# Performance work log

Hardware: AMD Instinct MI355X
Metric: run time of the kernel (lower is better)

Reference implementation:

```python
import jax, jax.numpy as jnp
import numpy as np
import math

B, S, D, H, K = 8, 4096, 1024, 16, 256
DK = D // H


def setup_inputs() -> dict:
    key = jax.random.key(0)
    ks = jax.random.split(key, 8)
    s = 1.0 / math.sqrt(D)
    x = jax.random.normal(ks[0], (B, S, D), dtype=jnp.float32)
    Wq = jax.random.normal(ks[1], (D, D), dtype=jnp.float32) * s
    Wk = jax.random.normal(ks[2], (D, D), dtype=jnp.float32) * s
    Wv = jax.random.normal(ks[3], (D, D), dtype=jnp.float32) * s
    Wo = jax.random.normal(ks[4], (D, D), dtype=jnp.float32) * s
    bq = jnp.zeros((D,), jnp.float32)
    bk = jnp.zeros((D,), jnp.float32)
    bv = jnp.zeros((D,), jnp.float32)
    bo = jnp.zeros((D,), jnp.float32)
    # xavier-uniform-style scale for the low-rank projections
    lim = math.sqrt(6.0 / (S + K))
    E = jax.random.uniform(ks[5], (S, K), jnp.float32, -lim, lim)
    Fp = jax.random.uniform(ks[6], (S, K), jnp.float32, -lim, lim)
    return {"x": x, "Wq": Wq, "bq": bq, "Wk": Wk, "bk": bk,
            "Wv": Wv, "bv": bv, "Wo": Wo, "bo": bo, "E": E, "Fp": Fp}


def reference(x, Wq, bq, Wk, bk, Wv, bv, Wo, bo, E, Fp):
    b, s, d = x.shape
    # QKV projections, split heads: [b, h, s, dk]
    def heads(y):
        return y.reshape(b, s, H, DK).transpose(0, 2, 1, 3)
    Q = heads(x @ Wq + bq)
    Kh = heads(x @ Wk + bk)
    Vh = heads(x @ Wv + bv)
    # Low-rank projection of K, V along sequence: [b, h, k, dk]
    Kp = jnp.einsum('sk,bhsd->bhkd', E, Kh)
    Vp = jnp.einsum('sk,bhsd->bhkd', Fp, Vh)
    # Attention over projected length k
    scores = jnp.einsum('bhsd,bhkd->bhsk', Q, Kp) / math.sqrt(DK)
    attn = jax.nn.softmax(scores, axis=-1)
    out = jnp.einsum('bhsk,bhkd->bhsd', attn, Vp)
    out = out.transpose(0, 2, 1, 3).reshape(b, s, d)
    return out @ Wo + bo
```

## Files before the change

### kernel.cpp

```cpp
#include <hip/hip_runtime.h>

#define AS1 __attribute__((address_space(1)))
#define AS3 __attribute__((address_space(3)))

typedef __attribute__((ext_vector_type(8))) short s16x8;
typedef __attribute__((ext_vector_type(4))) float f32x4;
typedef __attribute__((ext_vector_type(4))) unsigned short u16x4;
typedef __attribute__((ext_vector_type(8))) unsigned short u16x8;

#define MFMA16(a, b, c) __builtin_amdgcn_mfma_f32_16x16x32_bf16(a, b, c, 0, 0, 0)

static __device__ __forceinline__ unsigned short f2bf(float f) {
  unsigned u = __builtin_bit_cast(unsigned, f);
  u += 0x7fffu + ((u >> 16) & 1u);
  return (unsigned short)(u >> 16);
}

static __device__ __forceinline__ void gll16(const unsigned short* g, char* l) {
  __builtin_amdgcn_global_load_lds((const AS1 void*)g, (AS3 void*)l, 16, 0, 0);
}

#define BAR() asm volatile("s_barrier" ::: "memory")
#define WAITV(N) asm volatile("s_waitcnt vmcnt(" #N ")" ::: "memory")
#define FENCE() asm volatile("" ::: "memory")

__device__ __forceinline__ void gemm256_pipe(const unsigned short* __restrict__ A0, int lda,
                                             const unsigned short* __restrict__ B0, int ldb,
                                             int NT2, char* lds, f32x4 (&acc)[8][4]) {
  const int t = threadIdx.x;
  const int lane = t & 63, w = t >> 6, g = lane >> 4, l15 = lane & 15;
  const int wm = w >> 2, wn = w & 3;
  char* const A_lds[2] = {lds, lds + 65536};
  char* const B_lds[2] = {lds + 32768, lds + 98304};
  s16x8 af[2][4], bfr[2][4];

  const int rl = t >> 3, sl = t & 7;
  const unsigned short* aB = A0 + (size_t)rl * lda + ((sl ^ (rl & 7)) << 3);
  const unsigned short* bB = B0 + (size_t)rl * ldb + ((sl ^ (rl & 7)) << 3);
  const int woff = w << 10;

  char* pA[2][2];
  char* pB[2][2];
#pragma unroll
  for (int b = 0; b < 2; ++b)
#pragma unroll
    for (int kk = 0; kk < 2; ++kk) {
      pA[b][kk] = lds + b * 65536 + (wm * 64 + l15) * 128 + (((kk * 4 + g) ^ (l15 & 7)) << 4);
      pB[b][kk] = lds + 32768 + b * 65536 + (wn * 32 + l15) * 128 + (((kk * 4 + g) ^ (l15 & 7)) << 4);
    }

#define STGA(BUF, H, PTR)                                                                \
  do {                                                                                   \
    gll16((PTR) + (size_t)((H)*128) * lda, A_lds[BUF] + woff + (H)*16384);               \
    gll16((PTR) + (size_t)((H)*128 + 64) * lda, A_lds[BUF] + woff + (H)*16384 + 8192);   \
  } while (0)
#define STGB(BUF, H, PTR)                                                                \
  do {                                                                                   \
    gll16((PTR) + (size_t)((H)*128) * ldb, B_lds[BUF] + woff + (H)*16384);               \
    gll16((PTR) + (size_t)((H)*128 + 64) * ldb, B_lds[BUF] + woff + (H)*16384 + 8192);   \
  } while (0)

#define LDAQ(BUF, QH)                                                                    \
  do {                                                                                   \
    _Pragma("unroll") for (int mi = 0; mi < 4; ++mi)                                     \
        _Pragma("unroll") for (int kk = 0; kk < 2; ++kk)                                 \
            af[kk][mi] = *(const s16x8*)(pA[BUF][kk] + (QH)*16384 + mi * 2048);          \
  } while (0)
#define LDBP(BUF, NH)                                                                    \
  do {                                                                                   \
    _Pragma("unroll") for (int ni = 0; ni < 2; ++ni)                                     \
        _Pragma("unroll") for (int kk = 0; kk < 2; ++kk)                                 \
            bfr[kk][(NH)*2 + ni] =                                                       \
                *(const s16x8*)(pB[BUF][kk] + (NH)*16384 + ni * 2048);                   \
  } while (0)
#define MQUAD(QH, NH)                                                                    \
  do {                                                                                   \
    __builtin_amdgcn_s_setprio(1);                                                       \
    _Pragma("unroll") for (int kk = 0; kk < 2; ++kk)                                     \
        _Pragma("unroll") for (int mi = 0; mi < 4; ++mi)                                 \
            _Pragma("unroll") for (int ni = 0; ni < 2; ++ni)                             \
                acc[(QH)*4 + mi][(NH)*2 + ni] =                                          \
        MFMA16(af[kk][mi], bfr[kk][(NH)*2 + ni], acc[(QH)*4 + mi][(NH)*2 + ni]);         \
    __builtin_amdgcn_s_setprio(0);                                                       \
  } while (0)

  STGA(0, 0, aB);
  STGB(0, 0, bB);
  STGB(0, 1, bB);
  STGA(0, 1, aB);
  STGA(1, 0, aB + 64);
  STGB(1, 0, bB + 64);
  STGB(1, 1, bB + 64);
  STGA(1, 1, aB + 64);
  WAITV(8);
  BAR();

  for (int it = 0; it < NT2; ++it) {
    const bool pf = (it + 1 < NT2);
    const unsigned short* aN = aB + it * 128 + 128;
    const unsigned short* bN = bB + it * 128 + 128;
    LDAQ(0, 0);
    LDBP(0, 0);
    MQUAD(0, 0);
    BAR();
    LDBP(0, 1);
    if (pf) { STGA(0, 0, aN); STGB(0, 0, bN); }
    MQUAD(0, 1);
    BAR();
    LDAQ(0, 1);
    if (pf) STGB(0, 1, bN);
    MQUAD(1, 0);
    BAR();
    if (pf) STGA(0, 1, aN);
    MQUAD(1, 1);
    if (pf) WAITV(8);
    else WAITV(0);
    BAR();
    LDAQ(1, 0);
    LDBP(1, 0);
    MQUAD(0, 0);
    BAR();
    LDBP(1, 1);
    if (pf) { STGA(1, 0, aN + 64); STGB(1, 0, bN + 64); }
    MQUAD(0, 1);
    BAR();
    LDAQ(1, 1);
    if (pf) STGB(1, 1, bN + 64);
    MQUAD(1, 0);
    BAR();
    if (pf) STGA(1, 1, aN + 64);
    MQUAD(1, 1);
    if (pf) WAITV(8);
    BAR();
  }
#undef STGA
#undef STGB
#undef LDAQ
#undef LDBP
#undef MQUAD
}

__global__ __launch_bounds__(512, 2) void k_gemm_q(const unsigned short* __restrict__ xb,
                                                   const unsigned short* __restrict__ Wqt,
                                                   const float* __restrict__ biasq,
                                                   unsigned short* __restrict__ Qb) {
  __shared__ __align__(16) char lds[131072];
  f32x4 acc[8][4];
#pragma unroll
  for (int i = 0; i < 8; ++i)
#pragma unroll
    for (int j = 0; j < 4; ++j) acc[i][j] = f32x4{0.f, 0.f, 0.f, 0.f};
  int bid = blockIdx.y * 4 + blockIdx.x;
  bid = (bid & 7) * 64 + (bid >> 3);
  const int bn = bid & 3, bm = bid >> 2;
  gemm256_pipe(xb + (size_t)bm * 256 * 1024, 1024, Wqt + (size_t)bn * 256 * 1024, 1024, 8, lds, acc);

  const int t = threadIdx.x, lane = t & 63, w = t >> 6, g = lane >> 4, l15 = lane & 15;
  const int wm = w >> 2, wn = w & 3;
  const float QSC = 0.1803368801111204f;
#pragma unroll
  for (int nf = 0; nf < 4; ++nf) {
    const int n = bn * 256 + (nf >> 1) * 128 + wn * 32 + (nf & 1) * 16 + l15;
    const float bias = biasq[n];
#pragma unroll
    for (int mq = 0; mq < 8; ++mq) {
      const int m0 = bm * 256 + (mq >> 2) * 128 + wm * 64 + (mq & 3) * 16 + g * 4;
      const f32x4 v = acc[mq][nf];
#pragma unroll
      for (int r = 0; r < 4; ++r) Qb[(size_t)(m0 + r) * 1024 + n] = f2bf((v[r] + bias) * QSC);
    }
  }
}

__global__ __launch_bounds__(512, 2) void k_gemm_out(const unsigned short* __restrict__ AO,
                                                     const unsigned short* __restrict__ Wot,
                                                     const float* __restrict__ bo,
                                                     float* __restrict__ out) {
  __shared__ __align__(16) char lds[131072];
  f32x4 acc[8][4];
#pragma unroll
  for (int i = 0; i < 8; ++i)
#pragma unroll
    for (int j = 0; j < 4; ++j) acc[i][j] = f32x4{0.f, 0.f, 0.f, 0.f};
  int bid = blockIdx.y * 4 + blockIdx.x;
  bid = (bid & 7) * 64 + (bid >> 3);
  const int bn = bid & 3, bm = bid >> 2;
  gemm256_pipe(AO + (size_t)bm * 256 * 1024, 1024, Wot + (size_t)bn * 256 * 1024, 1024, 8, lds, acc);

  const int t = threadIdx.x, lane = t & 63, w = t >> 6, g = lane >> 4, l15 = lane & 15;
  const int wm = w >> 2, wn = w & 3;
#pragma unroll
  for (int nf = 0; nf < 4; ++nf) {
    const int n = bn * 256 + (nf >> 1) * 128 + wn * 32 + (nf & 1) * 16 + l15;
    const float bias = bo[n];
#pragma unroll
    for (int mq = 0; mq < 8; ++mq) {
      const int m0 = bm * 256 + (mq >> 2) * 128 + wm * 64 + (mq & 3) * 16 + g * 4;
      const f32x4 v = acc[mq][nf];
#pragma unroll
      for (int r = 0; r < 4; ++r) out[(size_t)(m0 + r) * 1024 + n] = v[r] + bias;
    }
  }
}

__device__ __forceinline__ void gemm_tile(const unsigned short* __restrict__ Ab, int lda,
                                          const unsigned short* __restrict__ Bb, int ldb,
                                          int Kc, char* lds, f32x4 (&acc)[4][4]) {
  const int t = threadIdx.x;
  const int lane = t & 63, w = t >> 6, g = lane >> 4, l15 = lane & 15;
  const int wm = w >> 1, wn = w & 1;
  char* As = lds;
  char* Bs = lds + 16384;
  for (int ks = 0; ks < Kc; ks += 64) {
    __syncthreads();
#pragma unroll
    for (int i = 0; i < 4; ++i) {
      const int c = i * 256 + t, row = c >> 3, sl = c & 7;
      const int col = ks + ((sl ^ (row & 7)) << 3);
      const int ubase = (i * 256 + w * 64) << 4;
      gll16(Ab + (size_t)row * lda + col, As + ubase);
      gll16(Bb + (size_t)row * ldb + col, Bs + ubase);
    }
    __syncthreads();
    s16x8 af[2][4], bfr[2][4];
#pragma unroll
    for (int kk = 0; kk < 2; ++kk)
#pragma unroll
      for (int x4 = 0; x4 < 4; ++x4) {
        const int ra = wm * 64 + x4 * 16 + l15;
        const int rb = wn * 64 + x4 * 16 + l15;
        af[kk][x4] = *(const s16x8*)(As + ra * 128 + ((((kk << 2) + g) ^ (ra & 7)) << 4));
        bfr[kk][x4] = *(const s16x8*)(Bs + rb * 128 + ((((kk << 2) + g) ^ (rb & 7)) << 4));
      }
#pragma unroll
    for (int kk = 0; kk < 2; ++kk)
#pragma unroll
      for (int mt = 0; mt < 4; ++mt)
#pragma unroll
        for (int nt = 0; nt < 4; ++nt)
          acc[mt][nt] = MFMA16(af[kk][mt], bfr[kk][nt], acc[mt][nt]);
  }
}

__global__ __launch_bounds__(256) void k_gemm_xef(const unsigned short* __restrict__ Et,
                                                  const unsigned short* __restrict__ Ft,
                                                  const unsigned short* __restrict__ xbT,
                                                  float* __restrict__ pxef) {
  __shared__ __align__(16) char lds[32768];
  f32x4 acc[4][4];
#pragma unroll
  for (int i = 0; i < 4; ++i)
#pragma unroll
    for (int j = 0; j < 4; ++j) acc[i][j] = f32x4{0.f, 0.f, 0.f, 0.f};
  const int z = blockIdx.z;
  const int ks = z >> 4, pair = z & 15, b = pair >> 1, ef = pair & 1;
  const unsigned short* Ab = (ef ? Ft : Et) + blockIdx.y * 128 * 4096 + ks * 1024;
  const unsigned short* Bb = xbT + (size_t)b * 4194304 + blockIdx.x * 128 * 4096 + ks * 1024;
  gemm_tile(Ab, 4096, Bb, 4096, 1024, lds, acc);

  const int t = threadIdx.x, lane = t & 63, w = t >> 6, g = lane >> 4, l15 = lane & 15;
  const int wm = w >> 1, wn = w & 1;
  const int nb = blockIdx.x * 128 + wn * 64, mb = blockIdx.y * 128 + wm * 64;
  float* C = pxef + (size_t)z * 262144;
#pragma unroll
  for (int nt = 0; nt < 4; ++nt) {
    const int n = nb + nt * 16 + l15;
#pragma unroll
    for (int mt = 0; mt < 4; ++mt) {
      const int m0 = mb + mt * 16 + g * 4;
      const f32x4 v = acc[mt][nt];
#pragma unroll
      for (int r = 0; r < 4; ++r) C[(m0 + r) * 1024 + n] = v[r];
    }
  }
}

__global__ __launch_bounds__(256) void k_xef_red(const float* __restrict__ pxef,
                                                 unsigned short* __restrict__ xEF) {
  const int j = (blockIdx.x * 256 + threadIdx.x) * 4;
  f32x4 s = *(const f32x4*)(pxef + j);
#pragma unroll
  for (int ks = 1; ks < 4; ++ks) {
    const f32x4 p = *(const f32x4*)(pxef + (size_t)ks * 4194304 + j);
#pragma unroll
    for (int r = 0; r < 4; ++r) s[r] += p[r];
  }
  u16x4 o;
#pragma unroll
  for (int r = 0; r < 4; ++r) o[r] = f2bf(s[r]);
  *(u16x4*)(xEF + j) = o;
}

__global__ __launch_bounds__(256) void k_kpvp2(const unsigned short* __restrict__ xEF,
                                               const unsigned short* __restrict__ Wqkvt,
                                               const float* __restrict__ biasq,
                                               const float* __restrict__ sEF,
                                               unsigned short* __restrict__ Kp,
                                               unsigned short* __restrict__ VpT) {
  __shared__ __align__(16) char lds[32768];
  f32x4 acc[4][4];
#pragma unroll
  for (int i = 0; i < 4; ++i)
#pragma unroll
    for (int j = 0; j < 4; ++j) acc[i][j] = f32x4{0.f, 0.f, 0.f, 0.f};
  const int b = blockIdx.z >> 1, kv = blockIdx.z & 1;
  const unsigned short* Ab = xEF + (size_t)(b * 2 + kv) * 262144 + blockIdx.y * 128 * 1024;
  const unsigned short* Bb = Wqkvt + (size_t)(1 + kv) * 1048576 + blockIdx.x * 128 * 1024;
  gemm_tile(Ab, 1024, Bb, 1024, 1024, lds, acc);

  const int t = threadIdx.x, lane = t & 63, w = t >> 6, g = lane >> 4, l15 = lane & 15;
  const int wm = w >> 1, wn = w & 1;
  const int nb = blockIdx.x * 128 + wn * 64, mb = blockIdx.y * 128 + wm * 64;
  const float* bias = biasq + (1 + kv) * 1024;
  const float* sE = sEF + kv * 256;
  if (!kv) {
    unsigned short* C = Kp + b * 262144;
#pragma unroll
    for (int nt = 0; nt < 4; ++nt) {
      const int n = nb + nt * 16 + l15;
      const float bn_ = bias[n];
#pragma unroll
      for (int mt = 0; mt < 4; ++mt) {
        const int m0 = mb + mt * 16 + g * 4;
        const f32x4 v = acc[mt][nt];
#pragma unroll
        for (int r = 0; r < 4; ++r) C[(m0 + r) * 1024 + n] = f2bf(v[r] + sE[m0 + r] * bn_);
      }
    }
  } else {
    unsigned short* C = VpT + b * 262144;
#pragma unroll
    for (int nt = 0; nt < 4; ++nt) {
      const int n = nb + nt * 16 + l15;
      const float bn_ = bias[n];
#pragma unroll
      for (int mt = 0; mt < 4; ++mt) {
        const int m0 = mb + mt * 16 + g * 4;
        const f32x4 v = acc[mt][nt];
        u16x4 pk;
#pragma unroll
        for (int r = 0; r < 4; ++r) pk[r] = f2bf(v[r] + sE[m0 + r] * bn_);
        *(u16x4*)(C + (n << 8) + m0) = pk;
      }
    }
  }
}

__global__ __launch_bounds__(512, 2) void k_attn(const unsigned short* __restrict__ Qb,
                                                 const unsigned short* __restrict__ Kp,
                                                 const unsigned short* __restrict__ VpT,
                                                 unsigned short* __restrict__ AO) {
  __shared__ __align__(16) char lds[131072];
  char* K0 = lds;
  char* V0 = lds + 32768;
  char* Qd = lds + 65536;
  char* Pb = lds + 98304;
  const int t = threadIdx.x, lane = t & 63, w = t >> 6, g = lane >> 4, l15 = lane & 15;
  const int sh = blockIdx.x, h = blockIdx.y, b = blockIdx.z;
  const int s0 = sh * 2048;
  const unsigned short* Qg = Qb + (size_t)(b * 4096 + s0) * 1024 + h * 64;
  const unsigned short* Kg = Kp + b * 262144 + h * 64;
  const unsigned short* Vg = VpT + b * 262144 + (h * 64) * 256;

#pragma unroll
  for (int i = 0; i < 4; ++i) {
    const int c = i * 512 + t, row = c >> 3, slr = c & 7;
    gll16(Kg + row * 1024 + ((slr ^ (row & 7)) << 3), K0 + ((i * 512 + w * 64) << 4));
  }
#pragma unroll
  for (int i = 0; i < 4; ++i) {
    const int c = i * 512 + t, row = c >> 5, slr = c & 31;
    gll16(Vg + row * 256 + ((slr ^ (row & 7)) << 3), V0 + ((i * 512 + w * 64) << 4));
  }
#pragma unroll
  for (int i = 0; i < 2; ++i) {
    const int c = i * 512 + t, row = c >> 3, slr = c & 7;
    gll16(Qg + row * 1024 + ((slr ^ (row & 7)) << 3), Qd + ((i * 512 + w * 64) << 4));
  }
  __syncthreads();

  char* const PwRow = Pb + (w << 12) + l15 * 256;
  const int wOffP = (g * 8 + l15 * 16) & 255;
  const int qrow = w * 16 + l15;
  const int qsw0 = (g ^ (qrow & 7)) << 4;
  const int qsw1 = ((4 + g) ^ (qrow & 7)) << 4;

  for (int st = 0; st < 16; ++st) {
    char* qb = Qd + ((st & 1) << 14);
    const s16x8 aq0 = *(const s16x8*)(qb + qrow * 128 + qsw0);
    const s16x8 aq1 = *(const s16x8*)(qb + qrow * 128 + qsw1);
    if (st < 15) {
      const unsigned short* Qn = Qg + (size_t)(st + 1) * 131072;
      char* qn = Qd + (((st + 1) & 1) << 14);
#pragma unroll
      for (int i = 0; i < 2; ++i) {
        const int c = i * 512 + t, row = c >> 3, slr = c & 7;
        gll16(Qn + row * 1024 + ((slr ^ (row & 7)) << 3), qn + ((i * 512 + w * 64) << 4));
      }
    }

    f32x4 sc[16];
#pragma unroll
    for (int nt = 0; nt < 16; ++nt) sc[nt] = f32x4{0.f, 0.f, 0.f, 0.f};
#pragma unroll
    for (int nt = 0; nt < 16; ++nt) {
      const int row = nt * 16 + l15;
      const s16x8 b0 = *(const s16x8*)(K0 + row * 128 + ((g ^ (row & 7)) << 4));
      const s16x8 b1 = *(const s16x8*)(K0 + row * 128 + (((4 + g) ^ (row & 7)) << 4));
      sc[nt] = MFMA16(b0, aq0, sc[nt]);
      sc[nt] = MFMA16(b1, aq1, sc[nt]);
    }

    float sm_ = 0.f;
    f32x4 ov[4];
#pragma unroll
    for (int nt = 0; nt < 4; ++nt) ov[nt] = f32x4{0.f, 0.f, 0.f, 0.f};

#pragma unroll
    for (int half = 0; half < 2; ++half) {
#pragma unroll
      for (int nt2 = 0; nt2 < 8; ++nt2) {
        const f32x4 s4 = sc[half * 8 + nt2];
        const float p0 = __builtin_amdgcn_exp2f(s4[0]);
        const float p1 = __builtin_amdgcn_exp2f(s4[1]);
        const float p2 = __builtin_amdgcn_exp2f(s4[2]);
        const float p3 = __builtin_amdgcn_exp2f(s4[3]);
        sm_ += (p0 + p1) + (p2 + p3);
        u16x4 pk;
        pk[0] = f2bf(p0);
        pk[1] = f2bf(p1);
        pk[2] = f2bf(p2);
        pk[3] = f2bf(p3);
        *(u16x4*)(PwRow + ((nt2 * 32 + wOffP) & 255)) = pk;
      }
      FENCE();
#pragma unroll
      for (int kk = 0; kk < 4; ++kk) {
        const int slh = ((kk * 4 + g + l15) & 15) << 4;
        const s16x8 ap = *(const s16x8*)(PwRow + slh);
#pragma unroll
        for (int nt = 0; nt < 4; ++nt) {
          const int rv = nt * 16 + l15;
          const int slot = half * 16 + (kk << 2) + g;
          const s16x8 bv = *(const s16x8*)(V0 + rv * 512 + ((slot ^ (rv & 7)) << 4));
          ov[nt] = MFMA16(ap, bv, ov[nt]);
        }
      }
      FENCE();
    }
    sm_ += __shfl_xor(sm_, 16);
    sm_ += __shfl_xor(sm_, 32);
    const float inv = 1.f / sm_;
    float invr[4];
#pragma unroll
    for (int r = 0; r < 4; ++r) invr[r] = __shfl(inv, (g << 2) + r);

    unsigned short* Ao = AO + (size_t)(b * 4096 + s0 + st * 128 + w * 16) * 1024 + h * 64;
#pragma unroll
    for (int nt = 0; nt < 4; ++nt) {
#pragma unroll
      for (int r = 0; r < 4; ++r) {
        Ao[(g * 4 + r) * 1024 + nt * 16 + l15] = f2bf(ov[nt][r] * invr[r]);
      }
    }
    __syncthreads();
  }
}

__global__ __launch_bounds__(256) void k_cvt_xt(const float* __restrict__ x,
                                                unsigned short* __restrict__ xb,
                                                unsigned short* __restrict__ xbT,
                                                const float* __restrict__ E,
                                                const float* __restrict__ Fp,
                                                float* __restrict__ part) {
  if (blockIdx.x >= 2048) {
    const int bb = blockIdx.x - 2048;
    const int sc = bb & 15, ef = bb >> 4, k = threadIdx.x;
    const float* M = ef ? Fp : E;
    float s = 0.f;
#pragma unroll 4
    for (int i = 0; i < 256; ++i) s += M[(size_t)((sc << 8) + i) * 256 + k];
    part[(ef * 16 + sc) * 256 + k] = s;
    return;
  }
  __shared__ unsigned short tl[256 * 72];
  const int t = threadIdx.x;
  const int stile = blockIdx.x >> 4, dt = blockIdx.x & 15;
  const int s0 = stile * 256, d0 = dt * 64;
  const int q = t >> 4, l15 = t & 15;

#pragma unroll
  for (int p = 0; p < 16; ++p) {
    const int row = p * 16 + q;
    const float4 v = *(const float4*)(x + (size_t)(s0 + row) * 1024 + d0 + l15 * 4);
    u16x4 o;
    o[0] = f2bf(v.x);
    o[1] = f2bf(v.y);
    o[2] = f2bf(v.z);
    o[3] = f2bf(v.w);
    *(u16x4*)(xb + (size_t)(s0 + row) * 1024 + d0 + l15 * 4) = o;
    *(u16x4*)(tl + row * 72 + ((l15 ^ p) << 2)) = o;
  }
  __syncthreads();

  u16x4 in[16];
#pragma unroll
  for (int i = 0; i < 16; ++i) {
    const int s = l15 * 16 + i;
    in[i] = *(const u16x4*)(tl + s * 72 + ((q ^ l15) << 2));
  }
  const int b = s0 >> 12, sb = s0 & 4095;
#pragma unroll
  for (int j = 0; j < 4; ++j) {
    u16x8 o0, o1;
#pragma unroll
    for (int i = 0; i < 8; ++i) {
      o0[i] = in[i][j];
      o1[i] = in[8 + i][j];
    }
    unsigned short* dst = xbT + (size_t)b * 4194304 + (size_t)(d0 + q * 4 + j) * 4096 + sb + l15 * 16;
    *(u16x8*)dst = o0;
    *(u16x8*)(dst + 8) = o1;
  }
}

__global__ __launch_bounds__(256) void k_prep(const float* __restrict__ Wq, const float* __restrict__ Wk,
                                              const float* __restrict__ Wv, const float* __restrict__ Wo,
                                              const float* __restrict__ E, const float* __restrict__ Fp,
                                              const float* __restrict__ bq, const float* __restrict__ bk,
                                              const float* __restrict__ bv,
                                              const float* __restrict__ part,
                                              unsigned short* __restrict__ Wqkvt, unsigned short* __restrict__ Wot,
                                              unsigned short* __restrict__ Et, unsigned short* __restrict__ Ft,
                                              float* __restrict__ biasq, float* __restrict__ sEF) {
  __shared__ unsigned short tl[256 * 72];
  const int bid = blockIdx.x, t = threadIdx.x;
  if (bid >= 384) {
    if (bid < 396) {
      const int j = (bid - 384) * 256 + t;
      biasq[j] = (j < 1024) ? bq[j] : (j < 2048 ? bk[j - 1024] : bv[j - 2048]);
    } else {
      const int j = (bid - 396) * 256 + t;
      const int ef = j >> 8, k = j & 255;
      float s = 0.f;
#pragma unroll
      for (int c = 0; c < 16; ++c) s += part[(ef * 16 + c) * 256 + k];
      sEF[j] = s;
    }
    return;
  }
  const float* src;
  unsigned short* dst;
  int srcld, dstld, s0, d0;
  if (bid < 256) {
    const int m = bid >> 6, tile = bid & 63;
    src = (m == 0) ? Wq : (m == 1) ? Wk : (m == 2) ? Wv : Wo;
    dst = (m < 3) ? (Wqkvt + m * 1048576) : Wot;
    srcld = 1024;
    dstld = 1024;
    s0 = (tile >> 4) * 256;
    d0 = (tile & 15) * 64;
  } else {
    const int j = bid - 256, ef = j >> 6, tile = j & 63;
    src = ef ? Fp : E;
    dst = ef ? Ft : Et;
    srcld = 256;
    dstld = 4096;
    s0 = (tile >> 2) * 256;
    d0 = (tile & 3) * 64;
  }
  const int q = t >> 4, l15 = t & 15;
#pragma unroll
  for (int p = 0; p < 16; ++p) {
    const int row = p * 16 + q;
    const float4 v = *(const float4*)(src + (size_t)(s0 + row) * srcld + d0 + l15 * 4);
    u16x4 o;
    o[0] = f2bf(v.x);
    o[1] = f2bf(v.y);
    o[2] = f2bf(v.z);
    o[3] = f2bf(v.w);
    *(u16x4*)(tl + row * 72 + ((l15 ^ p) << 2)) = o;
  }
  __syncthreads();
  u16x4 in[16];
#pragma unroll
  for (int i = 0; i < 16; ++i) {
    const int s = l15 * 16 + i;
    in[i] = *(const u16x4*)(tl + s * 72 + ((q ^ l15) << 2));
  }
#pragma unroll
  for (int j = 0; j < 4; ++j) {
    u16x8 o0, o1;
#pragma unroll
    for (int i = 0; i < 8; ++i) {
      o0[i] = in[i][j];
      o1[i] = in[8 + i][j];
    }
    unsigned short* dp = dst + (size_t)(d0 + q * 4 + j) * dstld + s0 + l15 * 16;
    *(u16x8*)dp = o0;
    *(u16x8*)(dp + 8) = o1;
  }
}

extern "C" void kernel_launch(void* const* d_in, const int* in_sizes, int n_in,
                              void* d_out, int out_size, void* d_ws, size_t ws_size,
                              hipStream_t stream) {
  const float* x = (const float*)d_in[0];
  const float* Wq = (const float*)d_in[1];
  const float* bq = (const float*)d_in[2];
  const float* Wk = (const float*)d_in[3];
  const float* bk = (const float*)d_in[4];
  const float* Wv = (const float*)d_in[5];
  const float* bv = (const float*)d_in[6];
  const float* Wo = (const float*)d_in[7];
  const float* bo = (const float*)d_in[8];
  const float* E = (const float*)d_in[9];
  const float* Fp = (const float*)d_in[10];

  char* ws = (char*)d_ws;
  size_t off = 0;
  auto alloc = [&](size_t bytes) {
    char* p = ws + off;
    off += (bytes + 255) & ~(size_t)255;
    return p;
  };
  unsigned short* xb = (unsigned short*)alloc(33554432ull * 2);
  unsigned short* xbT = (unsigned short*)alloc(33554432ull * 2);
  unsigned short* Qb = (unsigned short*)alloc(33554432ull * 2);
  unsigned short* Wqkvt = (unsigned short*)alloc(3145728ull * 2);
  unsigned short* Wot = (unsigned short*)alloc(1048576ull * 2);
  unsigned short* Et = (unsigned short*)alloc(1048576ull * 2);
  unsigned short* Ft = (unsigned short*)alloc(1048576ull * 2);
  unsigned short* xEF = (unsigned short*)alloc(4194304ull * 2);
  unsigned short* Kp = (unsigned short*)alloc(2097152ull * 2);
  unsigned short* VpT = (unsigned short*)alloc(2097152ull * 2);
  float* pxef = (float*)alloc(16777216ull * 4);
  float* biasq = (float*)alloc(3072 * 4);
  float* part = (float*)alloc(8192 * 4);
  float* sEF = (float*)alloc(512 * 4);
  (void)in_sizes; (void)n_in; (void)out_size; (void)ws_size;

  k_cvt_xt<<<2080, 256, 0, stream>>>(x, xb, xbT, E, Fp, part);
  k_prep<<<398, 256, 0, stream>>>(Wq, Wk, Wv, Wo, E, Fp, bq, bk, bv, part,
                                  Wqkvt, Wot, Et, Ft, biasq, sEF);
  k_gemm_q<<<dim3(4, 128), 512, 0, stream>>>(xb, Wqkvt, biasq, Qb);
  k_gemm_xef<<<dim3(8, 2, 64), 256, 0, stream>>>(Et, Ft, xbT, pxef);
  k_xef_red<<<4096, 256, 0, stream>>>(pxef, xEF);
  k_kpvp2<<<dim3(8, 2, 16), 256, 0, stream>>>(xEF, Wqkvt, biasq, sEF, Kp, VpT);
  k_attn<<<dim3(2, 16, 8), 512, 0, stream>>>(Qb, Kp, VpT, xb);
  k_gemm_out<<<dim3(4, 128), 512, 0, stream>>>(xb, Wot, bo, (float*)d_out);
}
```

Baseline: 400.8 us.

## Move xEF GEMM to 256x256 pipelined tile and fold E/F column sums into prep

The split-K E/F times x GEMM now uses the pipelined 256x256 tile routine with 512 threads instead of the simpler 128x128 tile loop. This cuts the block count from 1024 to 256 and raises reuse per block. The column sums of E and Fp are no longer partial sums computed in the conversion kernel and reduced in prep. Instead, two blocks in prep each loop over all 4096 rows. That removes the partial buffer and 32 blocks, but it serializes a long strided loop in only two blocks, which could lengthen prep.

```diff
diff --git a/kernel.cpp b/kernel.cpp
--- a/kernel.cpp
+++ b/kernel.cpp
@@ -140,6 +140,7 @@
 #undef MQUAD
 }
 
+
 __global__ __launch_bounds__(512, 2) void k_gemm_q(const unsigned short* __restrict__ xb,
                                                    const unsigned short* __restrict__ Wqt,
                                                    const float* __restrict__ biasq,
@@ -201,6 +202,54 @@
       for (int r = 0; r < 4; ++r) out[(size_t)(m0 + r) * 1024 + n] = v[r] + bias;
     }
   }
+}
+
+__global__ __launch_bounds__(512, 2) void k_gemm_xef(const unsigned short* __restrict__ Et,
+                                                     const unsigned short* __restrict__ Ft,
+                                                     const unsigned short* __restrict__ xbT,
+                                                     float* __restrict__ pxef) {
+  __shared__ __align__(16) char lds[131072];
+  f32x4 acc[8][4];
+#pragma unroll
+  for (int i = 0; i < 8; ++i)
+#pragma unroll
+    for (int j = 0; j < 4; ++j) acc[i][j] = f32x4{0.f, 0.f, 0.f, 0.f};
+  const int z = blockIdx.z;
+  const int ks = z >> 4, pair = z & 15, b = pair >> 1, ef = pair & 1;
+  const unsigned short* Ab = (ef ? Ft : Et) + ks * 1024;
+  const unsigned short* Bb = xbT + (size_t)b * 4194304 + (size_t)blockIdx.x * 256 * 4096 + ks * 1024;
+  gemm256_pipe(Ab, 4096, Bb, 4096, 8, lds, acc);
+
+  const int t = threadIdx.x, lane = t & 63, w = t >> 6, g = lane >> 4, l15 = lane & 15;
+  const int wm = w >> 2, wn = w & 3;
+  float* C = pxef + (size_t)z * 262144;
+#pragma unroll
+  for (int nf = 0; nf < 4; ++nf) {
+    const int n = blockIdx.x * 256 + (nf >> 1) * 128 + wn * 32 + (nf & 1) * 16 + l15;
+#pragma unroll
+    for (int mq = 0; mq < 8; ++mq) {
+      const int m0 = (mq >> 2) * 128 + wm * 64 + (mq & 3) * 16 + g * 4;
+      const f32x4 v = acc[mq][nf];
+#pragma unroll
+      for (int r = 0; r < 4; ++r) C[(size_t)(m0 + r) * 1024 + n] = v[r];
+    }
+  }
+}
+
+__global__ __launch_bounds__(256) void k_xef_red(const float* __restrict__ pxef,
+                                                 unsigned short* __restrict__ xEF) {
+  const int j = (blockIdx.x * 256 + threadIdx.x) * 4;
+  f32x4 s = *(const f32x4*)(pxef + j);
+#pragma unroll
+  for (int ks = 1; ks < 4; ++ks) {
+    const f32x4 p = *(const f32x4*)(pxef + (size_t)ks * 4194304 + j);
+#pragma unroll
+    for (int r = 0; r < 4; ++r) s[r] += p[r];
+  }
+  u16x4 o;
+#pragma unroll
+  for (int r = 0; r < 4; ++r) o[r] = f2bf(s[r]);
+  *(u16x4*)(xEF + j) = o;
 }
 
 __device__ __forceinline__ void gemm_tile(const unsigned short* __restrict__ Ab, int lda,
@@ -240,55 +289,6 @@
         for (int nt = 0; nt < 4; ++nt)
           acc[mt][nt] = MFMA16(af[kk][mt], bfr[kk][nt], acc[mt][nt]);
   }
-}
-
-__global__ __launch_bounds__(256) void k_gemm_xef(const unsigned short* __restrict__ Et,
-                                                  const unsigned short* __restrict__ Ft,
-                                                  const unsigned short* __restrict__ xbT,
-                                                  float* __restrict__ pxef) {
-  __shared__ __align__(16) char lds[32768];
-  f32x4 acc[4][4];
-#pragma unroll
-  for (int i = 0; i < 4; ++i)
-#pragma unroll
-    for (int j = 0; j < 4; ++j) acc[i][j] = f32x4{0.f, 0.f, 0.f, 0.f};
-  const int z = blockIdx.z;
-  const int ks = z >> 4, pair = z & 15, b = pair >> 1, ef = pair & 1;
-  const unsigned short* Ab = (ef ? Ft : Et) + blockIdx.y * 128 * 4096 + ks * 1024;
-  const unsigned short* Bb = xbT + (size_t)b * 4194304 + blockIdx.x * 128 * 4096 + ks * 1024;
-  gemm_tile(Ab, 4096, Bb, 4096, 1024, lds, acc);
-
-  const int t = threadIdx.x, lane = t & 63, w = t >> 6, g = lane >> 4, l15 = lane & 15;
-  const int wm = w >> 1, wn = w & 1;
-  const int nb = blockIdx.x * 128 + wn * 64, mb = blockIdx.y * 128 + wm * 64;
-  float* C = pxef + (size_t)z * 262144;
-#pragma unroll
-  for (int nt = 0; nt < 4; ++nt) {
-    const int n = nb + nt * 16 + l15;
-#pragma unroll
-    for (int mt = 0; mt < 4; ++mt) {
-      const int m0 = mb + mt * 16 + g * 4;
-      const f32x4 v = acc[mt][nt];
-#pragma unroll
-      for (int r = 0; r < 4; ++r) C[(m0 + r) * 1024 + n] = v[r];
-    }
-  }
-}
-
-__global__ __launch_bounds__(256) void k_xef_red(const float* __restrict__ pxef,
-                                                 unsigned short* __restrict__ xEF) {
-  const int j = (blockIdx.x * 256 + threadIdx.x) * 4;
-  f32x4 s = *(const f32x4*)(pxef + j);
-#pragma unroll
-  for (int ks = 1; ks < 4; ++ks) {
-    const f32x4 p = *(const f32x4*)(pxef + (size_t)ks * 4194304 + j);
-#pragma unroll
-    for (int r = 0; r < 4; ++r) s[r] += p[r];
-  }
-  u16x4 o;
-#pragma unroll
-  for (int r = 0; r < 4; ++r) o[r] = f2bf(s[r]);
-  *(u16x4*)(xEF + j) = o;
 }
 
 __global__ __launch_bounds__(256) void k_kpvp2(const unsigned short* __restrict__ xEF,
@@ -469,20 +469,7 @@
 
 __global__ __launch_bounds__(256) void k_cvt_xt(const float* __restrict__ x,
                                                 unsigned short* __restrict__ xb,
-                                                unsigned short* __restrict__ xbT,
-                                                const float* __restrict__ E,
-                                                const float* __restrict__ Fp,
-                                                float* __restrict__ part) {
-  if (blockIdx.x >= 2048) {
-    const int bb = blockIdx.x - 2048;
-    const int sc = bb & 15, ef = bb >> 4, k = threadIdx.x;
-    const float* M = ef ? Fp : E;
-    float s = 0.f;
-#pragma unroll 4
-    for (int i = 0; i < 256; ++i) s += M[(size_t)((sc << 8) + i) * 256 + k];
-    part[(ef * 16 + sc) * 256 + k] = s;
-    return;
-  }
+                                                unsigned short* __restrict__ xbT) {
   __shared__ unsigned short tl[256 * 72];
   const int t = threadIdx.x;
   const int stile = blockIdx.x >> 4, dt = blockIdx.x & 15;
@@ -529,7 +516,6 @@
                                               const float* __restrict__ E, const float* __restrict__ Fp,
                                               const float* __restrict__ bq, const float* __restrict__ bk,
                                               const float* __restrict__ bv,
-                                              const float* __restrict__ part,
                                               unsigned short* __restrict__ Wqkvt, unsigned short* __restrict__ Wot,
                                               unsigned short* __restrict__ Et, unsigned short* __restrict__ Ft,
                                               float* __restrict__ biasq, float* __restrict__ sEF) {
@@ -540,12 +526,12 @@
       const int j = (bid - 384) * 256 + t;
       biasq[j] = (j < 1024) ? bq[j] : (j < 2048 ? bk[j - 1024] : bv[j - 2048]);
     } else {
-      const int j = (bid - 396) * 256 + t;
-      const int ef = j >> 8, k = j & 255;
+      const int ef = bid - 396, k = t;
+      const float* M = ef ? Fp : E;
       float s = 0.f;
-#pragma unroll
-      for (int c = 0; c < 16; ++c) s += part[(ef * 16 + c) * 256 + k];
-      sEF[j] = s;
+#pragma unroll 4
+      for (int i = 0; i < 4096; ++i) s += M[(size_t)i * 256 + k];
+      sEF[ef * 256 + k] = s;
     }
     return;
   }
@@ -636,15 +622,14 @@
   unsigned short* VpT = (unsigned short*)alloc(2097152ull * 2);
   float* pxef = (float*)alloc(16777216ull * 4);
   float* biasq = (float*)alloc(3072 * 4);
-  float* part = (float*)alloc(8192 * 4);
   float* sEF = (float*)alloc(512 * 4);
   (void)in_sizes; (void)n_in; (void)out_size; (void)ws_size;
 
-  k_cvt_xt<<<2080, 256, 0, stream>>>(x, xb, xbT, E, Fp, part);
-  k_prep<<<398, 256, 0, stream>>>(Wq, Wk, Wv, Wo, E, Fp, bq, bk, bv, part,
+  k_cvt_xt<<<2048, 256, 0, stream>>>(x, xb, xbT);
+  k_prep<<<398, 256, 0, stream>>>(Wq, Wk, Wv, Wo, E, Fp, bq, bk, bv,
                                   Wqkvt, Wot, Et, Ft, biasq, sEF);
   k_gemm_q<<<dim3(4, 128), 512, 0, stream>>>(xb, Wqkvt, biasq, Qb);
-  k_gemm_xef<<<dim3(8, 2, 64), 256, 0, stream>>>(Et, Ft, xbT, pxef);
+  k_gemm_xef<<<dim3(4, 1, 64), 512, 0, stream>>>(Et, Ft, xbT, pxef);
   k_xef_red<<<4096, 256, 0, stream>>>(pxef, xEF);
   k_kpvp2<<<dim3(8, 2, 16), 256, 0, stream>>>(xEF, Wqkvt, biasq, sEF, Kp, VpT);
   k_attn<<<dim3(2, 16, 8), 512, 0, stream>>>(Qb, Kp, VpT, xb);
```

New measurement: 601.7 us. 50.1% more time.
